# Kernel optimization log

Measured on AMD Instinct MI355X. Metric: run time of the kernel, lower is better.

## Reference

```python
import jax, jax.numpy as jnp
import numpy as np

D = 8192

def setup_inputs() -> dict:
    key = jax.random.key(0)
    k0, k1, k2 = jax.random.split(key, 3)
    x0 = jax.random.normal(k0, (D,), dtype=jnp.float32)
    x = jax.random.normal(k1, (D,), dtype=jnp.float32)
    weight = jax.random.normal(k2, (D,), dtype=jnp.float32)
    bias = jnp.zeros((D,), dtype=jnp.float32)
    return {"x0": x0, "x": x, "weight": weight, "bias": bias}

def reference(x0, x, weight, bias):
    # Literal math: outer(w, x) @ x0 + bias + x.
    # outer(w, x) is [D, D]; matvec with x0 gives [D].
    cross = jnp.outer(weight, x) @ x0
    return cross + bias + x
```

## Files before the change

### kernel.cpp

```cpp
#include <hip/hip_runtime.h>


#define D 8192
#define NTHREADS 1024

__global__ __launch_bounds__(NTHREADS) void cross_layer_kernel(
    const float* __restrict__ x0,
    const float* __restrict__ x,
    const float* __restrict__ weight,
    const float* __restrict__ bias,
    float* __restrict__ out) {

    const int tid = threadIdx.x;

    const float4* __restrict__ x04 = (const float4*)x0;
    const float4* __restrict__ x4  = (const float4*)x;
    const float4* __restrict__ w4  = (const float4*)weight;
    const float4* __restrict__ b4  = (const float4*)bias;
    float4* __restrict__ o4        = (float4*)out;

    float4 xa0 = x04[tid];
    float4 xa1 = x04[tid + NTHREADS];
    float4 xb0 = x4[tid];
    float4 xb1 = x4[tid + NTHREADS];

    float p = xa0.x * xb0.x + xa0.y * xb0.y + xa0.z * xb0.z + xa0.w * xb0.w
            + xa1.x * xb1.x + xa1.y * xb1.y + xa1.z * xb1.z + xa1.w * xb1.w;

    #pragma unroll
    for (int off = 32; off > 0; off >>= 1) {
        p += __shfl_down(p, off, 64);
    }

    __shared__ float s_wave[NTHREADS / 64];
    __shared__ float s_dot;
    const int lane = tid & 63;
    const int wave = tid >> 6;
    if (lane == 0) s_wave[wave] = p;
    __syncthreads();

    if (tid == 0) {
        float d = 0.0f;
        #pragma unroll
        for (int i = 0; i < NTHREADS / 64; ++i) d += s_wave[i];
        s_dot = d;
    }
    __syncthreads();
    const float dot = s_dot;

    float4 wv0 = w4[tid];
    float4 wv1 = w4[tid + NTHREADS];
    float4 bv0 = b4[tid];
    float4 bv1 = b4[tid + NTHREADS];

    float4 r0, r1;
    r0.x = fmaf(wv0.x, dot, bv0.x + xb0.x);
    r0.y = fmaf(wv0.y, dot, bv0.y + xb0.y);
    r0.z = fmaf(wv0.z, dot, bv0.z + xb0.z);
    r0.w = fmaf(wv0.w, dot, bv0.w + xb0.w);
    r1.x = fmaf(wv1.x, dot, bv1.x + xb1.x);
    r1.y = fmaf(wv1.y, dot, bv1.y + xb1.y);
    r1.z = fmaf(wv1.z, dot, bv1.z + xb1.z);
    r1.w = fmaf(wv1.w, dot, bv1.w + xb1.w);

    o4[tid] = r0;
    o4[tid + NTHREADS] = r1;
}

extern "C" void kernel_launch(void* const* d_in, const int* in_sizes, int n_in,
                              void* d_out, int out_size, void* d_ws, size_t ws_size,
                              hipStream_t stream) {
    const float* x0     = (const float*)d_in[0];
    const float* x      = (const float*)d_in[1];
    const float* weight = (const float*)d_in[2];
    const float* bias   = (const float*)d_in[3];
    float* out          = (float*)d_out;

    cross_layer_kernel<<<1, NTHREADS, 0, stream>>>(x0, x, weight, bias, out);
}
```

Baseline: 59.43 us.

## Spread output across 32 blocks with redundant per-block dot product

Replaces the single 1024-thread block with 32 blocks of 256 threads. Each block recomputes the full x0·x dot product itself, then writes its own 256-element slice of the output. This spreads the load and store traffic across many compute units instead of one. In exchange, the dot-product reads are repeated 32 times, though those reads will mostly hit in cache.

```diff
diff --git a/kernel.cpp b/kernel.cpp
--- a/kernel.cpp
+++ b/kernel.cpp
@@ -2,7 +2,9 @@
 
 
 #define D 8192
-#define NTHREADS 1024
+#define NTHREADS 256
+#define NBLOCKS (D / NTHREADS)
+#define F4_PER_THREAD ((D / 4) / NTHREADS)
 
 __global__ __launch_bounds__(NTHREADS) void cross_layer_kernel(
     const float* __restrict__ x0,
@@ -12,20 +14,29 @@
     float* __restrict__ out) {
 
     const int tid = threadIdx.x;
+    const int gid = blockIdx.x * NTHREADS + tid;
 
     const float4* __restrict__ x04 = (const float4*)x0;
     const float4* __restrict__ x4  = (const float4*)x;
-    const float4* __restrict__ w4  = (const float4*)weight;
-    const float4* __restrict__ b4  = (const float4*)bias;
-    float4* __restrict__ o4        = (float4*)out;
 
-    float4 xa0 = x04[tid];
-    float4 xa1 = x04[tid + NTHREADS];
-    float4 xb0 = x4[tid];
-    float4 xb1 = x4[tid + NTHREADS];
+    float4 a[F4_PER_THREAD];
+    float4 b[F4_PER_THREAD];
+    #pragma unroll
+    for (int k = 0; k < F4_PER_THREAD; ++k) {
+        a[k] = x04[tid + k * NTHREADS];
+        b[k] = x4[tid + k * NTHREADS];
+    }
 
-    float p = xa0.x * xb0.x + xa0.y * xb0.y + xa0.z * xb0.z + xa0.w * xb0.w
-            + xa1.x * xb1.x + xa1.y * xb1.y + xa1.z * xb1.z + xa1.w * xb1.w;
+    const float wi = weight[gid];
+    const float bi = bias[gid];
+    const float xi = x[gid];
+
+    float p = 0.0f;
+    #pragma unroll
+    for (int k = 0; k < F4_PER_THREAD; ++k) {
+        p += a[k].x * b[k].x + a[k].y * b[k].y
+           + a[k].z * b[k].z + a[k].w * b[k].w;
+    }
 
     #pragma unroll
     for (int off = 32; off > 0; off >>= 1) {
@@ -38,33 +49,13 @@
     const int wave = tid >> 6;
     if (lane == 0) s_wave[wave] = p;
     __syncthreads();
-
     if (tid == 0) {
-        float d = 0.0f;
-        #pragma unroll
-        for (int i = 0; i < NTHREADS / 64; ++i) d += s_wave[i];
-        s_dot = d;
+        s_dot = s_wave[0] + s_wave[1] + s_wave[2] + s_wave[3];
     }
     __syncthreads();
     const float dot = s_dot;
 
-    float4 wv0 = w4[tid];
-    float4 wv1 = w4[tid + NTHREADS];
-    float4 bv0 = b4[tid];
-    float4 bv1 = b4[tid + NTHREADS];
-
-    float4 r0, r1;
-    r0.x = fmaf(wv0.x, dot, bv0.x + xb0.x);
-    r0.y = fmaf(wv0.y, dot, bv0.y + xb0.y);
-    r0.z = fmaf(wv0.z, dot, bv0.z + xb0.z);
-    r0.w = fmaf(wv0.w, dot, bv0.w + xb0.w);
-    r1.x = fmaf(wv1.x, dot, bv1.x + xb1.x);
-    r1.y = fmaf(wv1.y, dot, bv1.y + xb1.y);
-    r1.z = fmaf(wv1.z, dot, bv1.z + xb1.z);
-    r1.w = fmaf(wv1.w, dot, bv1.w + xb1.w);
-
-    o4[tid] = r0;
-    o4[tid + NTHREADS] = r1;
+    out[gid] = fmaf(wi, dot, bi + xi);
 }
 
 extern "C" void kernel_launch(void* const* d_in, const int* in_sizes, int n_in,
@@ -76,5 +67,5 @@
     const float* bias   = (const float*)d_in[3];
     float* out          = (float*)d_out;
 
-    cross_layer_kernel<<<1, NTHREADS, 0, stream>>>(x0, x, weight, bias, out);
+    cross_layer_kernel<<<NBLOCKS, NTHREADS, 0, stream>>>(x0, x, weight, bias, out);
 }
```

Result: no change. 59.42 us (-0.0%).
